# Kernel optimization log

Measured on AMD Instinct MI355X. Metric: run time of the kernel, lower is better.

## Reference

```python
import jax, jax.numpy as jnp
import numpy as np

N = 100000      # nodes
E = 1600000     # edges (avg degree 16)
D_IN, D_H, D_OUT = 128, 128, 64
NORM_SCALE = 1.0
EPS = 1e-6


def setup_inputs() -> dict:
    key = jax.random.key(0)
    ks = jax.random.split(key, 9)
    x = jax.random.normal(ks[0], (N, D_IN), dtype=jnp.float32)
    edge_index = jax.random.randint(ks[1], (2, E), 0, N, dtype=jnp.int32)
    edge_weight = jax.random.uniform(ks[2], (E,), dtype=jnp.float32)
    # GraphConv = Linear then spmm(adj, .); Glorot-ish init for weights
    W0 = jax.random.normal(ks[3], (D_IN, D_H), dtype=jnp.float32) / np.float32(np.sqrt(D_IN))
    b0 = jnp.zeros((D_H,), jnp.float32)
    W1 = jax.random.normal(ks[4], (D_H, D_H), dtype=jnp.float32) / np.float32(np.sqrt(D_H))
    b1 = jnp.zeros((D_H,), jnp.float32)
    Wout = jax.random.normal(ks[5], (D_H, D_OUT), dtype=jnp.float32) / np.float32(np.sqrt(D_H))
    bout = jnp.zeros((D_OUT,), jnp.float32)
    return {"x": x, "edge_index": edge_index, "edge_weight": edge_weight,
            "W0": W0, "b0": b0, "W1": W1, "b1": b1, "Wout": Wout, "bout": bout}


def _pair_norm(h):
    # PairNorm mode 'PN': center columns, divide by sqrt(mean squared row norm)
    h = h - jnp.mean(h, axis=0, keepdims=True)
    rownorm_mean = jnp.sqrt(EPS + jnp.mean(jnp.sum(h * h, axis=1)))
    return NORM_SCALE * h / rownorm_mean


def reference(x, edge_index, edge_weight, W0, b0, W1, b1, Wout, bout):
    src = edge_index[0]
    dst = edge_index[1]

    def graph_conv(h, W, b):
        h = h @ W + b                              # [N, d_out]
        msg = edge_weight[:, None] * h[src]        # [E, d_out] gather
        return jax.ops.segment_sum(msg, dst, num_segments=N)  # spmm(adj, h)

    x_old = jnp.zeros((), jnp.float32)
    for (W, b) in ((W0, b0), (W1, b1)):
        # dropout p=0 -> identity (omitted)
        h = graph_conv(x, W, b)
        h = jax.nn.relu(_pair_norm(h))
        x = h + x_old        # residual=1 -> skip every layer
        x_old = x
    return graph_conv(x, Wout, bout)
```

## Files before the change

### kernel.cpp

```cpp
#include <hip/hip_runtime.h>

#define N_NODES 100000
#define N_EDGES 1600000
#define DH 128
#define DOUT 64
#define EPS 1e-6f
#define NBINS 8
#define BINW 12500
#define NREP 64

typedef __attribute__((ext_vector_type(8))) short s8v;
typedef __attribute__((ext_vector_type(4))) float f32x4;

__device__ inline unsigned bfround(float f) {
    unsigned u = __float_as_uint(f);
    return (u + 0x7fffu + ((u >> 16) & 1u)) >> 16;
}
__device__ inline unsigned pack2(float a, float b) { return bfround(a) | (bfround(b) << 16); }
__device__ inline float blo(unsigned u) { return __uint_as_float(u << 16); }
__device__ inline float bhi(unsigned u) { return __uint_as_float(u & 0xffff0000u); }

template <int COLS, int PN>
__global__ __launch_bounds__(256) void gemm_mfma(const float* __restrict__ Xa,
                                                 const float* __restrict__ muA,
                                                 const float* __restrict__ invA,
                                                 const float* __restrict__ Xb,
                                                 const float* __restrict__ muB,
                                                 const float* __restrict__ invB,
                                                 const float* __restrict__ W,
                                                 const float* __restrict__ bias,
                                                 unsigned* __restrict__ Y, int nrows) {
    constexpr int CT = COLS / 16;
    __shared__ unsigned wtu[COLS][64];
    __shared__ unsigned xbu[64][64];

    const int tid = threadIdx.x;
    const int wv = tid >> 6;
    const int lane = tid & 63;
    const float sA = (PN >= 1) ? invA[0] : 0.f;
    const float sB = (PN == 2) ? invB[0] : 0.f;

    {
        ushort* wts = (ushort*)wtu;
        constexpr int NV4 = 128 * COLS / 4;
        for (int i = tid; i < NV4; i += 256) {
            int k = i / (COLS / 4);
            int c4 = i % (COLS / 4);
            float4 w4 = reinterpret_cast<const float4*>(W)[i];
            float vals[4] = {w4.x, w4.y, w4.z, w4.w};
            int u = k >> 1, kb = k & 1;
#pragma unroll
            for (int j = 0; j < 4; ++j) {
                int c = c4 * 4 + j;
                int us = u ^ ((c & 7) << 2);
                wts[c * 128 + us * 2 + kb] = (ushort)bfround(vals[j]);
            }
        }
    }

    float bv[CT];
#pragma unroll
    for (int f = 0; f < CT; ++f) bv[f] = bias[f * 16 + (lane & 15)];

    const int row0 = blockIdx.x * 128;
    const int myr = (wv << 4) + (lane & 15);

#pragma unroll
    for (int ms = 0; ms < 2; ++ms) {
        const int rb = row0 + ms * 64;
        __syncthreads();
        for (int i = tid; i < 2048; i += 256) {
            int r = i >> 5;
            int c4 = i & 31;
            float4 v = make_float4(0.f, 0.f, 0.f, 0.f);
            if (rb + r < nrows) {
                v = reinterpret_cast<const float4*>(Xa + (size_t)(rb + r) * 128)[c4];
                if constexpr (PN >= 1) {
                    float4 m = reinterpret_cast<const float4*>(muA)[c4];
                    v.x = fmaxf((v.x - m.x) * sA, 0.f);
                    v.y = fmaxf((v.y - m.y) * sA, 0.f);
                    v.z = fmaxf((v.z - m.z) * sA, 0.f);
                    v.w = fmaxf((v.w - m.w) * sA, 0.f);
                }
                if constexpr (PN == 2) {
                    float4 v2 = reinterpret_cast<const float4*>(Xb + (size_t)(rb + r) * 128)[c4];
                    float4 m2 = reinterpret_cast<const float4*>(muB)[c4];
                    v.x += fmaxf((v2.x - m2.x) * sB, 0.f);
                    v.y += fmaxf((v2.y - m2.y) * sB, 0.f);
                    v.z += fmaxf((v2.z - m2.z) * sB, 0.f);
                    v.w += fmaxf((v2.w - m2.w) * sB, 0.f);
                }
            }
            int sw = (r & 7) << 2;
            xbu[r][(c4 * 2) ^ sw] = pack2(v.x, v.y);
            xbu[r][(c4 * 2 + 1) ^ sw] = pack2(v.z, v.w);
        }
        __syncthreads();

        f32x4 acc[CT];
#pragma unroll
        for (int f = 0; f < CT; ++f) acc[f] = (f32x4){0.f, 0.f, 0.f, 0.f};
        const int xsw = (myr & 7) << 2;
#pragma unroll
        for (int kc = 0; kc < 4; ++kc) {
            const int u0 = kc * 16 + (lane >> 4) * 4;
            s8v a = *reinterpret_cast<const s8v*>(&xbu[myr][u0 ^ xsw]);
#pragma unroll
            for (int f = 0; f < CT; ++f) {
                const int c = f * 16 + (lane & 15);
                s8v b = *reinterpret_cast<const s8v*>(&wtu[c][u0 ^ ((c & 7) << 2)]);
                acc[f] = __builtin_amdgcn_mfma_f32_16x16x32_bf16(a, b, acc[f], 0, 0, 0);
            }
        }

#pragma unroll
        for (int f = 0; f < CT; ++f) {
#pragma unroll
            for (int r = 0; r < 4; ++r) {
                float v = acc[f][r] + bv[f];
                float p = __shfl_xor(v, 1, 64);
                unsigned pk = (lane & 1) ? pack2(p, v) : pack2(v, p);
                int grow = rb + (wv << 4) + ((lane >> 4) << 2) + r;
                if (grow < nrows && ((lane & 1) == (f & 1))) {
                    Y[(size_t)grow * (COLS / 2) + f * 8 + ((lane & 15) >> 1)] = pk;
                }
            }
        }
    }
}

__global__ __launch_bounds__(256) void hist_kernel(const int* __restrict__ dst,
                                                   int* __restrict__ counts) {
    int i = blockIdx.x * blockDim.x + threadIdx.x;
    const int stride = gridDim.x * blockDim.x;
    for (; i < N_EDGES / 4; i += stride) {
        int4 d = reinterpret_cast<const int4*>(dst)[i];
        atomicAdd(&counts[d.x], 1);
        atomicAdd(&counts[d.y], 1);
        atomicAdd(&counts[d.z], 1);
        atomicAdd(&counts[d.w], 1);
    }
}

__global__ __launch_bounds__(1024) void scan_kernel(const int* __restrict__ counts,
                                                    int* __restrict__ rowptr) {
    __shared__ int wsum[16];
    const int tid = threadIdx.x;
    const int lane = tid & 63;
    const int w = tid >> 6;
    int offset = 0;
    if (tid == 0) rowptr[0] = 0;
    for (int base = 0; base < N_NODES; base += 4096) {
        int i = base + tid * 4;
        int4 v = make_int4(0, 0, 0, 0);
        if (i < N_NODES) v = *reinterpret_cast<const int4*>(counts + i);
        int p0 = v.x, p1 = p0 + v.y, p2 = p1 + v.z, p3 = p2 + v.w;
        int incl = p3;
#pragma unroll
        for (int d = 1; d < 64; d <<= 1) {
            int t = __shfl_up(incl, d, 64);
            if (lane >= d) incl += t;
        }
        if (lane == 63) wsum[w] = incl;
        __syncthreads();
        if (w == 0 && lane < 16) {
            int t = wsum[lane];
#pragma unroll
            for (int d = 1; d < 16; d <<= 1) {
                int u = __shfl_up(t, d, 64);
                if (lane >= d) t += u;
            }
            wsum[lane] = t;
        }
        __syncthreads();
        int woff = (w == 0) ? 0 : wsum[w - 1];
        int chunk_total = wsum[15];
        int tbase = offset + woff + incl - p3;
        if (i < N_NODES) {
            rowptr[i + 1] = tbase + p0;
            rowptr[i + 2] = tbase + p1;
            rowptr[i + 3] = tbase + p2;
            rowptr[i + 4] = tbase + p3;
        }
        offset += chunk_total;
        __syncthreads();
    }
}

__global__ __launch_bounds__(256) void bucket_kernel(const int* __restrict__ src,
                                                     const int* __restrict__ dst,
                                                     const float* __restrict__ ew,
                                                     const int* __restrict__ rowptr,
                                                     int* __restrict__ fill,
                                                     int2* __restrict__ em) {
    const int myBin = blockIdx.x & (NBINS - 1);
    const int lo = myBin * BINW;
    const int hi = lo + BINW;
    int e = (blockIdx.x >> 3) * 256 + threadIdx.x;
    const int stride = (gridDim.x >> 3) * 256;
    for (; e < N_EDGES; e += stride) {
        int d = dst[e];
        if (d >= lo && d < hi) {
            int pos = atomicAdd(&fill[d], 1);
            em[rowptr[d] + pos] = make_int2(src[e], __float_as_int(ew[e]));
        }
    }
}

__global__ __launch_bounds__(256) void agg128b_kernel(const unsigned* __restrict__ Hb,
                                                      const int* __restrict__ rowptr,
                                                      const int2* __restrict__ em,
                                                      float* __restrict__ B,
                                                      float* __restrict__ cs_part,
                                                      float* __restrict__ ss_part) {
    __shared__ int2 smeta[4][64];
    __shared__ float cs[4][128];
    __shared__ float ssw[4];
    const int wv = threadIdx.x >> 6;
    const int lane = threadIdx.x & 63;
    const int node = blockIdx.x * 4 + wv;
    const int beg = rowptr[node];
    const int end = rowptr[node + 1];
    const int2* sm = smeta[wv];
    float ax0 = 0.f, ay0 = 0.f, ax1 = 0.f, ay1 = 0.f;

    for (int c = beg; c < end; c += 64) {
        smeta[wv][lane] = (c + lane < end) ? em[c + lane] : make_int2(0, 0);
        const int cnt = min(64, end - c);
        const int rounds = (cnt + 7) >> 3;
        for (int g = 0; g < rounds; ++g) {
            int2 m0 = sm[g * 8 + 0];
            int2 m1 = sm[g * 8 + 1];
            int2 m2 = sm[g * 8 + 2];
            int2 m3 = sm[g * 8 + 3];
            int2 m4 = sm[g * 8 + 4];
            int2 m5 = sm[g * 8 + 5];
            int2 m6 = sm[g * 8 + 6];
            int2 m7 = sm[g * 8 + 7];
            unsigned u0 = Hb[(size_t)m0.x * 64 + lane];
            unsigned u1 = Hb[(size_t)m1.x * 64 + lane];
            unsigned u2 = Hb[(size_t)m2.x * 64 + lane];
            unsigned u3 = Hb[(size_t)m3.x * 64 + lane];
            unsigned u4 = Hb[(size_t)m4.x * 64 + lane];
            unsigned u5 = Hb[(size_t)m5.x * 64 + lane];
            unsigned u6 = Hb[(size_t)m6.x * 64 + lane];
            unsigned u7 = Hb[(size_t)m7.x * 64 + lane];
            float w0 = __int_as_float(m0.y), w1 = __int_as_float(m1.y);
            float w2 = __int_as_float(m2.y), w3 = __int_as_float(m3.y);
            float w4 = __int_as_float(m4.y), w5 = __int_as_float(m5.y);
            float w6 = __int_as_float(m6.y), w7 = __int_as_float(m7.y);
            ax0 += w0 * blo(u0); ay0 += w0 * bhi(u0);
            ax1 += w1 * blo(u1); ay1 += w1 * bhi(u1);
            ax0 += w2 * blo(u2); ay0 += w2 * bhi(u2);
            ax1 += w3 * blo(u3); ay1 += w3 * bhi(u3);
            ax0 += w4 * blo(u4); ay0 += w4 * bhi(u4);
            ax1 += w5 * blo(u5); ay1 += w5 * bhi(u5);
            ax0 += w6 * blo(u6); ay0 += w6 * bhi(u6);
            ax1 += w7 * blo(u7); ay1 += w7 * bhi(u7);
        }
    }
    float2 acc = make_float2(ax0 + ax1, ay0 + ay1);
    reinterpret_cast<float2*>(B + (size_t)node * DH)[lane] = acc;

    cs[wv][lane * 2] = acc.x;
    cs[wv][lane * 2 + 1] = acc.y;
    float sq = acc.x * acc.x + acc.y * acc.y;
#pragma unroll
    for (int off = 32; off; off >>= 1) sq += __shfl_down(sq, off, 64);
    if (lane == 0) ssw[wv] = sq;
    __syncthreads();
    const int rep = blockIdx.x & (NREP - 1);
    if (threadIdx.x < 128) {
        float s = cs[0][threadIdx.x] + cs[1][threadIdx.x] + cs[2][threadIdx.x] + cs[3][threadIdx.x];
        atomicAdd(&cs_part[rep * 128 + threadIdx.x], s);
    }
    if (threadIdx.x == 0) atomicAdd(&ss_part[rep], ssw[0] + ssw[1] + ssw[2] + ssw[3]);
}

__global__ __launch_bounds__(256) void agg64b_kernel(const unsigned* __restrict__ Hb,
                                                     const int* __restrict__ rowptr,
                                                     const int2* __restrict__ em,
                                                     float* __restrict__ out) {
    __shared__ int2 smeta[4][64];
    const int wv = threadIdx.x >> 6;
    const int lane = threadIdx.x & 63;
    const int half = lane >> 5;
    const int col = lane & 31;
    const int node = blockIdx.x * 4 + wv;
    const int beg = rowptr[node];
    const int end = rowptr[node + 1];
    const int2* sm = smeta[wv];
    float ax0 = 0.f, ay0 = 0.f, ax1 = 0.f, ay1 = 0.f;

    for (int c = beg; c < end; c += 64) {
        smeta[wv][lane] = (c + lane < end) ? em[c + lane] : make_int2(0, 0);
        const int cnt = min(64, end - c);
        const int rounds = (cnt + 15) >> 4;
        for (int g = 0; g < rounds; ++g) {
            const int b = g * 16 + half;
            int2 m0 = sm[b + 0];
            int2 m1 = sm[b + 2];
            int2 m2 = sm[b + 4];
            int2 m3 = sm[b + 6];
            int2 m4 = sm[b + 8];
            int2 m5 = sm[b + 10];
            int2 m6 = sm[b + 12];
            int2 m7 = sm[b + 14];
            unsigned u0 = Hb[(size_t)m0.x * 32 + col];
            unsigned u1 = Hb[(size_t)m1.x * 32 + col];
            unsigned u2 = Hb[(size_t)m2.x * 32 + col];
            unsigned u3 = Hb[(size_t)m3.x * 32 + col];
            unsigned u4 = Hb[(size_t)m4.x * 32 + col];
            unsigned u5 = Hb[(size_t)m5.x * 32 + col];
            unsigned u6 = Hb[(size_t)m6.x * 32 + col];
            unsigned u7 = Hb[(size_t)m7.x * 32 + col];
            float w0 = __int_as_float(m0.y), w1 = __int_as_float(m1.y);
            float w2 = __int_as_float(m2.y), w3 = __int_as_float(m3.y);
            float w4 = __int_as_float(m4.y), w5 = __int_as_float(m5.y);
            float w6 = __int_as_float(m6.y), w7 = __int_as_float(m7.y);
            ax0 += w0 * blo(u0); ay0 += w0 * bhi(u0);
            ax1 += w1 * blo(u1); ay1 += w1 * bhi(u1);
            ax0 += w2 * blo(u2); ay0 += w2 * bhi(u2);
            ax1 += w3 * blo(u3); ay1 += w3 * bhi(u3);
            ax0 += w4 * blo(u4); ay0 += w4 * bhi(u4);
            ax1 += w5 * blo(u5); ay1 += w5 * bhi(u5);
            ax0 += w6 * blo(u6); ay0 += w6 * bhi(u6);
            ax1 += w7 * blo(u7); ay1 += w7 * bhi(u7);
        }
    }
    float ax = ax0 + ax1, ay = ay0 + ay1;
    ax += __shfl_xor(ax, 32, 64);
    ay += __shfl_xor(ay, 32, 64);
    if (lane < 32) {
        reinterpret_cast<float2*>(out + (size_t)node * DOUT)[col] = make_float2(ax, ay);
    }
}

__global__ void finalize_stats(const float* __restrict__ cs_part,
                               const float* __restrict__ ss_part, float* __restrict__ mu,
                               float* __restrict__ inv) {
    const int t = threadIdx.x;
    float m = 0.f;
    for (int r = 0; r < NREP; ++r) m += cs_part[r * 128 + t];
    float mean = m / (float)N_NODES;
    mu[t] = mean;
    float v = mean * mean;
    __shared__ float partl[2];
    __shared__ float sstot;
#pragma unroll
    for (int off = 32; off; off >>= 1) v += __shfl_down(v, off, 64);
    if ((t & 63) == 0) partl[t >> 6] = v;
    float ss = (t < NREP) ? ss_part[t] : 0.f;
#pragma unroll
    for (int off = 32; off; off >>= 1) ss += __shfl_down(ss, off, 64);
    if (t == 0) sstot = ss;
    __syncthreads();
    if (t == 0) {
        float musq = partl[0] + partl[1];
        float s = (sstot - (float)N_NODES * musq) / (float)N_NODES;
        inv[0] = rsqrtf(EPS + s);
    }
}

extern "C" void kernel_launch(void* const* d_in, const int* in_sizes, int n_in,
                              void* d_out, int out_size, void* d_ws, size_t ws_size,
                              hipStream_t stream) {
    const float* x = (const float*)d_in[0];
    const int* edge_index = (const int*)d_in[1];
    const float* ew = (const float*)d_in[2];
    const float* W0 = (const float*)d_in[3];
    const float* b0 = (const float*)d_in[4];
    const float* W1 = (const float*)d_in[5];
    const float* b1 = (const float*)d_in[6];
    const float* Wout = (const float*)d_in[7];
    const float* bout = (const float*)d_in[8];

    const int* src = edge_index;
    const int* dst = edge_index + N_EDGES;
    float* out = (float*)d_out;

    float* base = (float*)d_ws;
    unsigned* Hb = (unsigned*)base;
    float* B1 = base + (size_t)N_NODES * 64;
    float* B2 = B1 + (size_t)N_NODES * DH;
    int2* em = (int2*)(B2 + (size_t)N_NODES * DH);
    int* counts = (int*)(em + N_EDGES);
    int* fill = counts + N_NODES;
    int* rowptr = fill + N_NODES;
    size_t soff = (size_t)(rowptr + N_NODES + 1 - (int*)base);
    soff = (soff + 3) & ~(size_t)3;
    float* stats = base + soff;
    float* cs_part1 = stats;
    float* ss_part1 = cs_part1 + NREP * 128;
    float* cs_part2 = ss_part1 + NREP;
    float* ss_part2 = cs_part2 + NREP * 128;
    float* mu1 = ss_part2 + NREP;
    float* inv1 = mu1 + 128;
    float* mu2 = inv1 + 4;
    float* inv2 = mu2 + 128;

    const int gemm_grid = (N_NODES + 127) / 128;
    const int agg_grid = N_NODES / 4;

    hipMemsetAsync(counts, 0, (size_t)2 * N_NODES * sizeof(int), stream);
    hipMemsetAsync(stats, 0, (size_t)2 * (NREP * 128 + NREP) * sizeof(float), stream);

    hist_kernel<<<1024, 256, 0, stream>>>(dst, counts);
    scan_kernel<<<1, 1024, 0, stream>>>(counts, rowptr);
    bucket_kernel<<<2048, 256, 0, stream>>>(src, dst, ew, rowptr, fill, em);

    gemm_mfma<128, 0><<<gemm_grid, 256, 0, stream>>>(
        x, nullptr, nullptr, nullptr, nullptr, nullptr, W0, b0, Hb, N_NODES);
    agg128b_kernel<<<agg_grid, 256, 0, stream>>>(Hb, rowptr, em, B1, cs_part1, ss_part1);
    finalize_stats<<<1, 128, 0, stream>>>(cs_part1, ss_part1, mu1, inv1);

    gemm_mfma<128, 1><<<gemm_grid, 256, 0, stream>>>(
        B1, mu1, inv1, nullptr, nullptr, nullptr, W1, b1, Hb, N_NODES);
    agg128b_kernel<<<agg_grid, 256, 0, stream>>>(Hb, rowptr, em, B2, cs_part2, ss_part2);
    finalize_stats<<<1, 128, 0, stream>>>(cs_part2, ss_part2, mu2, inv2);

    gemm_mfma<64, 2><<<gemm_grid, 256, 0, stream>>>(
        B2, mu2, inv2, B1, mu1, inv1, Wout, bout, Hb, N_NODES);
    agg64b_kernel<<<agg_grid, 256, 0, stream>>>(Hb, rowptr, em, out);
}
```

Baseline: 556.7 us.

## Store aggregated hidden features as bf16 and widen gather loads in aggregation kernels

The intermediate aggregation outputs B1/B2 are now written as packed bf16 instead of fp32, and the following GEMMs read bf16 and unpack them while applying PairNorm. This halves the bytes written by the 128-wide aggregation and read back by the next GEMMs. The aggregation kernels also switch to 8-byte uint2 gathers, so each lane handles four columns and the edge list is split across wave halves or quarters, followed by a shuffle reduction. The cost is extra rounding of intermediates to bf16, with slightly lower accuracy, and per-node stats are still computed from the fp32 accumulators.

After: 539.4 us. 1.03x faster.

```diff
diff --git a/kernel.cpp b/kernel.cpp
--- a/kernel.cpp
+++ b/kernel.cpp
@@ -21,10 +21,10 @@
 __device__ inline float bhi(unsigned u) { return __uint_as_float(u & 0xffff0000u); }
 
 template <int COLS, int PN>
-__global__ __launch_bounds__(256) void gemm_mfma(const float* __restrict__ Xa,
+__global__ __launch_bounds__(256) void gemm_mfma(const void* __restrict__ Xav,
                                                  const float* __restrict__ muA,
                                                  const float* __restrict__ invA,
-                                                 const float* __restrict__ Xb,
+                                                 const unsigned* __restrict__ Xbu2,
                                                  const float* __restrict__ muB,
                                                  const float* __restrict__ invB,
                                                  const float* __restrict__ W,
@@ -69,31 +69,56 @@
     for (int ms = 0; ms < 2; ++ms) {
         const int rb = row0 + ms * 64;
         __syncthreads();
-        for (int i = tid; i < 2048; i += 256) {
-            int r = i >> 5;
-            int c4 = i & 31;
-            float4 v = make_float4(0.f, 0.f, 0.f, 0.f);
-            if (rb + r < nrows) {
-                v = reinterpret_cast<const float4*>(Xa + (size_t)(rb + r) * 128)[c4];
-                if constexpr (PN >= 1) {
-                    float4 m = reinterpret_cast<const float4*>(muA)[c4];
-                    v.x = fmaxf((v.x - m.x) * sA, 0.f);
-                    v.y = fmaxf((v.y - m.y) * sA, 0.f);
-                    v.z = fmaxf((v.z - m.z) * sA, 0.f);
-                    v.w = fmaxf((v.w - m.w) * sA, 0.f);
+        if constexpr (PN == 0) {
+            const float* Xa = (const float*)Xav;
+            for (int i = tid; i < 2048; i += 256) {
+                int r = i >> 5;
+                int c4 = i & 31;
+                float4 v = make_float4(0.f, 0.f, 0.f, 0.f);
+                if (rb + r < nrows) v = reinterpret_cast<const float4*>(Xa + (size_t)(rb + r) * 128)[c4];
+                int sw = (r & 7) << 2;
+                xbu[r][(c4 * 2) ^ sw] = pack2(v.x, v.y);
+                xbu[r][(c4 * 2 + 1) ^ sw] = pack2(v.z, v.w);
+            }
+        } else {
+            const unsigned* Xa = (const unsigned*)Xav;
+            for (int i = tid; i < 1024; i += 256) {
+                int r = i >> 4;
+                int c4 = i & 15;
+                float v0 = 0.f, v1 = 0.f, v2 = 0.f, v3 = 0.f, v4 = 0.f, v5 = 0.f, v6 = 0.f,
+                      v7 = 0.f;
+                if (rb + r < nrows) {
+                    uint4 uv = reinterpret_cast<const uint4*>(Xa + (size_t)(rb + r) * 64)[c4];
+                    float4 ma = reinterpret_cast<const float4*>(muA)[c4 * 2];
+                    float4 mb = reinterpret_cast<const float4*>(muA)[c4 * 2 + 1];
+                    v0 = fmaxf((blo(uv.x) - ma.x) * sA, 0.f);
+                    v1 = fmaxf((bhi(uv.x) - ma.y) * sA, 0.f);
+                    v2 = fmaxf((blo(uv.y) - ma.z) * sA, 0.f);
+                    v3 = fmaxf((bhi(uv.y) - ma.w) * sA, 0.f);
+                    v4 = fmaxf((blo(uv.z) - mb.x) * sA, 0.f);
+                    v5 = fmaxf((bhi(uv.z) - mb.y) * sA, 0.f);
+                    v6 = fmaxf((blo(uv.w) - mb.z) * sA, 0.f);
+                    v7 = fmaxf((bhi(uv.w) - mb.w) * sA, 0.f);
+                    if constexpr (PN == 2) {
+                        uint4 u2 = reinterpret_cast<const uint4*>(Xbu2 + (size_t)(rb + r) * 64)[c4];
+                        float4 na = reinterpret_cast<const float4*>(muB)[c4 * 2];
+                        float4 nb = reinterpret_cast<const float4*>(muB)[c4 * 2 + 1];
+                        v0 += fmaxf((blo(u2.x) - na.x) * sB, 0.f);
+                        v1 += fmaxf((bhi(u2.x) - na.y) * sB, 0.f);
+                        v2 += fmaxf((blo(u2.y) - na.z) * sB, 0.f);
+                        v3 += fmaxf((bhi(u2.y) - na.w) * sB, 0.f);
+                        v4 += fmaxf((blo(u2.z) - nb.x) * sB, 0.f);
+                        v5 += fmaxf((bhi(u2.z) - nb.y) * sB, 0.f);
+                        v6 += fmaxf((blo(u2.w) - nb.z) * sB, 0.f);
+                        v7 += fmaxf((bhi(u2.w) - nb.w) * sB, 0.f);
+                    }
                 }
-                if constexpr (PN == 2) {
-                    float4 v2 = reinterpret_cast<const float4*>(Xb + (size_t)(rb + r) * 128)[c4];
-                    float4 m2 = reinterpret_cast<const float4*>(muB)[c4];
-                    v.x += fmaxf((v2.x - m2.x) * sB, 0.f);
-                    v.y += fmaxf((v2.y - m2.y) * sB, 0.f);
-                    v.z += fmaxf((v2.z - m2.z) * sB, 0.f);
-                    v.w += fmaxf((v2.w - m2.w) * sB, 0.f);
-                }
-            }
-            int sw = (r & 7) << 2;
-            xbu[r][(c4 * 2) ^ sw] = pack2(v.x, v.y);
-            xbu[r][(c4 * 2 + 1) ^ sw] = pack2(v.z, v.w);
+                int sw = (r & 7) << 2;
+                xbu[r][(c4 * 4 + 0) ^ sw] = pack2(v0, v1);
+                xbu[r][(c4 * 4 + 1) ^ sw] = pack2(v2, v3);
+                xbu[r][(c4 * 4 + 2) ^ sw] = pack2(v4, v5);
+                xbu[r][(c4 * 4 + 3) ^ sw] = pack2(v6, v7);
+            }
         }
         __syncthreads();
 
@@ -210,7 +235,7 @@
 __global__ __launch_bounds__(256) void agg128b_kernel(const unsigned* __restrict__ Hb,
                                                       const int* __restrict__ rowptr,
                                                       const int2* __restrict__ em,
-                                                      float* __restrict__ B,
+                                                      unsigned* __restrict__ Bb,
                                                       float* __restrict__ cs_part,
                                                       float* __restrict__ ss_part) {
     __shared__ int2 smeta[4][64];
@@ -218,79 +243,13 @@
     __shared__ float ssw[4];
     const int wv = threadIdx.x >> 6;
     const int lane = threadIdx.x & 63;
+    const int half = lane >> 5;
+    const int col2 = lane & 31;
     const int node = blockIdx.x * 4 + wv;
     const int beg = rowptr[node];
     const int end = rowptr[node + 1];
     const int2* sm = smeta[wv];
-    float ax0 = 0.f, ay0 = 0.f, ax1 = 0.f, ay1 = 0.f;
-
-    for (int c = beg; c < end; c += 64) {
-        smeta[wv][lane] = (c + lane < end) ? em[c + lane] : make_int2(0, 0);
-        const int cnt = min(64, end - c);
-        const int rounds = (cnt + 7) >> 3;
-        for (int g = 0; g < rounds; ++g) {
-            int2 m0 = sm[g * 8 + 0];
-            int2 m1 = sm[g * 8 + 1];
-            int2 m2 = sm[g * 8 + 2];
-            int2 m3 = sm[g * 8 + 3];
-            int2 m4 = sm[g * 8 + 4];
-            int2 m5 = sm[g * 8 + 5];
-            int2 m6 = sm[g * 8 + 6];
-            int2 m7 = sm[g * 8 + 7];
-            unsigned u0 = Hb[(size_t)m0.x * 64 + lane];
-            unsigned u1 = Hb[(size_t)m1.x * 64 + lane];
-            unsigned u2 = Hb[(size_t)m2.x * 64 + lane];
-            unsigned u3 = Hb[(size_t)m3.x * 64 + lane];
-            unsigned u4 = Hb[(size_t)m4.x * 64 + lane];
-            unsigned u5 = Hb[(size_t)m5.x * 64 + lane];
-            unsigned u6 = Hb[(size_t)m6.x * 64 + lane];
-            unsigned u7 = Hb[(size_t)m7.x * 64 + lane];
-            float w0 = __int_as_float(m0.y), w1 = __int_as_float(m1.y);
-            float w2 = __int_as_float(m2.y), w3 = __int_as_float(m3.y);
-            float w4 = __int_as_float(m4.y), w5 = __int_as_float(m5.y);
-            float w6 = __int_as_float(m6.y), w7 = __int_as_float(m7.y);
-            ax0 += w0 * blo(u0); ay0 += w0 * bhi(u0);
-            ax1 += w1 * blo(u1); ay1 += w1 * bhi(u1);
-            ax0 += w2 * blo(u2); ay0 += w2 * bhi(u2);
-            ax1 += w3 * blo(u3); ay1 += w3 * bhi(u3);
-            ax0 += w4 * blo(u4); ay0 += w4 * bhi(u4);
-            ax1 += w5 * blo(u5); ay1 += w5 * bhi(u5);
-            ax0 += w6 * blo(u6); ay0 += w6 * bhi(u6);
-            ax1 += w7 * blo(u7); ay1 += w7 * bhi(u7);
-        }
-    }
-    float2 acc = make_float2(ax0 + ax1, ay0 + ay1);
-    reinterpret_cast<float2*>(B + (size_t)node * DH)[lane] = acc;
-
-    cs[wv][lane * 2] = acc.x;
-    cs[wv][lane * 2 + 1] = acc.y;
-    float sq = acc.x * acc.x + acc.y * acc.y;
-#pragma unroll
-    for (int off = 32; off; off >>= 1) sq += __shfl_down(sq, off, 64);
-    if (lane == 0) ssw[wv] = sq;
-    __syncthreads();
-    const int rep = blockIdx.x & (NREP - 1);
-    if (threadIdx.x < 128) {
-        float s = cs[0][threadIdx.x] + cs[1][threadIdx.x] + cs[2][threadIdx.x] + cs[3][threadIdx.x];
-        atomicAdd(&cs_part[rep * 128 + threadIdx.x], s);
-    }
-    if (threadIdx.x == 0) atomicAdd(&ss_part[rep], ssw[0] + ssw[1] + ssw[2] + ssw[3]);
-}
-
-__global__ __launch_bounds__(256) void agg64b_kernel(const unsigned* __restrict__ Hb,
-                                                     const int* __restrict__ rowptr,
-                                                     const int2* __restrict__ em,
-                                                     float* __restrict__ out) {
-    __shared__ int2 smeta[4][64];
-    const int wv = threadIdx.x >> 6;
-    const int lane = threadIdx.x & 63;
-    const int half = lane >> 5;
-    const int col = lane & 31;
-    const int node = blockIdx.x * 4 + wv;
-    const int beg = rowptr[node];
-    const int end = rowptr[node + 1];
-    const int2* sm = smeta[wv];
-    float ax0 = 0.f, ay0 = 0.f, ax1 = 0.f, ay1 = 0.f;
+    float a0 = 0.f, a1 = 0.f, a2 = 0.f, a3 = 0.f;
 
     for (int c = beg; c < end; c += 64) {
         smeta[wv][lane] = (c + lane < end) ? em[c + lane] : make_int2(0, 0);
@@ -306,33 +265,115 @@
             int2 m5 = sm[b + 10];
             int2 m6 = sm[b + 12];
             int2 m7 = sm[b + 14];
-            unsigned u0 = Hb[(size_t)m0.x * 32 + col];
-            unsigned u1 = Hb[(size_t)m1.x * 32 + col];
-            unsigned u2 = Hb[(size_t)m2.x * 32 + col];
-            unsigned u3 = Hb[(size_t)m3.x * 32 + col];
-            unsigned u4 = Hb[(size_t)m4.x * 32 + col];
-            unsigned u5 = Hb[(size_t)m5.x * 32 + col];
-            unsigned u6 = Hb[(size_t)m6.x * 32 + col];
-            unsigned u7 = Hb[(size_t)m7.x * 32 + col];
+            uint2 u0 = *reinterpret_cast<const uint2*>(Hb + (size_t)m0.x * 64 + col2 * 2);
+            uint2 u1 = *reinterpret_cast<const uint2*>(Hb + (size_t)m1.x * 64 + col2 * 2);
+            uint2 u2 = *reinterpret_cast<const uint2*>(Hb + (size_t)m2.x * 64 + col2 * 2);
+            uint2 u3 = *reinterpret_cast<const uint2*>(Hb + (size_t)m3.x * 64 + col2 * 2);
+            uint2 u4 = *reinterpret_cast<const uint2*>(Hb + (size_t)m4.x * 64 + col2 * 2);
+            uint2 u5 = *reinterpret_cast<const uint2*>(Hb + (size_t)m5.x * 64 + col2 * 2);
+            uint2 u6 = *reinterpret_cast<const uint2*>(Hb + (size_t)m6.x * 64 + col2 * 2);
+            uint2 u7 = *reinterpret_cast<const uint2*>(Hb + (size_t)m7.x * 64 + col2 * 2);
             float w0 = __int_as_float(m0.y), w1 = __int_as_float(m1.y);
             float w2 = __int_as_float(m2.y), w3 = __int_as_float(m3.y);
             float w4 = __int_as_float(m4.y), w5 = __int_as_float(m5.y);
             float w6 = __int_as_float(m6.y), w7 = __int_as_float(m7.y);
-            ax0 += w0 * blo(u0); ay0 += w0 * bhi(u0);
-            ax1 += w1 * blo(u1); ay1 += w1 * bhi(u1);
-            ax0 += w2 * blo(u2); ay0 += w2 * bhi(u2);
-            ax1 += w3 * blo(u3); ay1 += w3 * bhi(u3);
-            ax0 += w4 * blo(u4); ay0 += w4 * bhi(u4);
-            ax1 += w5 * blo(u5); ay1 += w5 * bhi(u5);
-            ax0 += w6 * blo(u6); ay0 += w6 * bhi(u6);
-            ax1 += w7 * blo(u7); ay1 += w7 * bhi(u7);
-        }
-    }
-    float ax = ax0 + ax1, ay = ay0 + ay1;
-    ax += __shfl_xor(ax, 32, 64);
-    ay += __shfl_xor(ay, 32, 64);
+            a0 += w0 * blo(u0.x); a1 += w0 * bhi(u0.x); a2 += w0 * blo(u0.y); a3 += w0 * bhi(u0.y);
+            a0 += w1 * blo(u1.x); a1 += w1 * bhi(u1.x); a2 += w1 * blo(u1.y); a3 += w1 * bhi(u1.y);
+            a0 += w2 * blo(u2.x); a1 += w2 * bhi(u2.x); a2 += w2 * blo(u2.y); a3 += w2 * bhi(u2.y);
+            a0 += w3 * blo(u3.x); a1 += w3 * bhi(u3.x); a2 += w3 * blo(u3.y); a3 += w3 * bhi(u3.y);
+            a0 += w4 * blo(u4.x); a1 += w4 * bhi(u4.x); a2 += w4 * blo(u4.y); a3 += w4 * bhi(u4.y);
+            a0 += w5 * blo(u5.x); a1 += w5 * bhi(u5.x); a2 += w5 * blo(u5.y); a3 += w5 * bhi(u5.y);
+            a0 += w6 * blo(u6.x); a1 += w6 * bhi(u6.x); a2 += w6 * blo(u6.y); a3 += w6 * bhi(u6.y);
+            a0 += w7 * blo(u7.x); a1 += w7 * bhi(u7.x); a2 += w7 * blo(u7.y); a3 += w7 * bhi(u7.y);
+        }
+    }
+    a0 += __shfl_xor(a0, 32, 64);
+    a1 += __shfl_xor(a1, 32, 64);
+    a2 += __shfl_xor(a2, 32, 64);
+    a3 += __shfl_xor(a3, 32, 64);
+
+    float sq = 0.f;
     if (lane < 32) {
-        reinterpret_cast<float2*>(out + (size_t)node * DOUT)[col] = make_float2(ax, ay);
+        uint2 op;
+        op.x = pack2(a0, a1);
+        op.y = pack2(a2, a3);
+        *reinterpret_cast<uint2*>(Bb + (size_t)node * 64 + col2 * 2) = op;
+        cs[wv][col2 * 4 + 0] = a0;
+        cs[wv][col2 * 4 + 1] = a1;
+        cs[wv][col2 * 4 + 2] = a2;
+        cs[wv][col2 * 4 + 3] = a3;
+        sq = a0 * a0 + a1 * a1 + a2 * a2 + a3 * a3;
+    }
+#pragma unroll
+    for (int off = 32; off; off >>= 1) sq += __shfl_down(sq, off, 64);
+    if (lane == 0) ssw[wv] = sq;
+    __syncthreads();
+    const int rep = blockIdx.x & (NREP - 1);
+    if (threadIdx.x < 128) {
+        float s = cs[0][threadIdx.x] + cs[1][threadIdx.x] + cs[2][threadIdx.x] + cs[3][threadIdx.x];
+        atomicAdd(&cs_part[rep * 128 + threadIdx.x], s);
+    }
+    if (threadIdx.x == 0) atomicAdd(&ss_part[rep], ssw[0] + ssw[1] + ssw[2] + ssw[3]);
+}
+
+__global__ __launch_bounds__(256) void agg64b_kernel(const unsigned* __restrict__ Hb,
+                                                     const int* __restrict__ rowptr,
+                                                     const int2* __restrict__ em,
+                                                     float* __restrict__ out) {
+    __shared__ int2 smeta[4][64];
+    const int wv = threadIdx.x >> 6;
+    const int lane = threadIdx.x & 63;
+    const int q = lane >> 4;
+    const int col2 = lane & 15;
+    const int node = blockIdx.x * 4 + wv;
+    const int beg = rowptr[node];
+    const int end = rowptr[node + 1];
+    const int2* sm = smeta[wv];
+    float a0 = 0.f, a1 = 0.f, a2 = 0.f, a3 = 0.f;
+
+    for (int c = beg; c < end; c += 64) {
+        smeta[wv][lane] = (c + lane < end) ? em[c + lane] : make_int2(0, 0);
+        const int cnt = min(64, end - c);
+        const int rounds = (cnt + 31) >> 5;
+        for (int g = 0; g < rounds; ++g) {
+            const int b = g * 32 + q;
+            int2 m0 = sm[b + 0];
+            int2 m1 = sm[b + 4];
+            int2 m2 = sm[b + 8];
+            int2 m3 = sm[b + 12];
+            int2 m4 = sm[b + 16];
+            int2 m5 = sm[b + 20];
+            int2 m6 = sm[b + 24];
+            int2 m7 = sm[b + 28];
+            uint2 u0 = *reinterpret_cast<const uint2*>(Hb + (size_t)m0.x * 32 + col2 * 2);
+            uint2 u1 = *reinterpret_cast<const uint2*>(Hb + (size_t)m1.x * 32 + col2 * 2);
+            uint2 u2 = *reinterpret_cast<const uint2*>(Hb + (size_t)m2.x * 32 + col2 * 2);
+            uint2 u3 = *reinterpret_cast<const uint2*>(Hb + (size_t)m3.x * 32 + col2 * 2);
+            uint2 u4 = *reinterpret_cast<const uint2*>(Hb + (size_t)m4.x * 32 + col2 * 2);
+            uint2 u5 = *reinterpret_cast<const uint2*>(Hb + (size_t)m5.x * 32 + col2 * 2);
+            uint2 u6 = *reinterpret_cast<const uint2*>(Hb + (size_t)m6.x * 32 + col2 * 2);
+            uint2 u7 = *reinterpret_cast<const uint2*>(Hb + (size_t)m7.x * 32 + col2 * 2);
+            float w0 = __int_as_float(m0.y), w1 = __int_as_float(m1.y);
+            float w2 = __int_as_float(m2.y), w3 = __int_as_float(m3.y);
+            float w4 = __int_as_float(m4.y), w5 = __int_as_float(m5.y);
+            float w6 = __int_as_float(m6.y), w7 = __int_as_float(m7.y);
+            a0 += w0 * blo(u0.x); a1 += w0 * bhi(u0.x); a2 += w0 * blo(u0.y); a3 += w0 * bhi(u0.y);
+            a0 += w1 * blo(u1.x); a1 += w1 * bhi(u1.x); a2 += w1 * blo(u1.y); a3 += w1 * bhi(u1.y);
+            a0 += w2 * blo(u2.x); a1 += w2 * bhi(u2.x); a2 += w2 * blo(u2.y); a3 += w2 * bhi(u2.y);
+            a0 += w3 * blo(u3.x); a1 += w3 * bhi(u3.x); a2 += w3 * blo(u3.y); a3 += w3 * bhi(u3.y);
+            a0 += w4 * blo(u4.x); a1 += w4 * bhi(u4.x); a2 += w4 * blo(u4.y); a3 += w4 * bhi(u4.y);
+            a0 += w5 * blo(u5.x); a1 += w5 * bhi(u5.x); a2 += w5 * blo(u5.y); a3 += w5 * bhi(u5.y);
+            a0 += w6 * blo(u6.x); a1 += w6 * bhi(u6.x); a2 += w6 * blo(u6.y); a3 += w6 * bhi(u6.y);
+            a0 += w7 * blo(u7.x); a1 += w7 * bhi(u7.x); a2 += w7 * blo(u7.y); a3 += w7 * bhi(u7.y);
+        }
+    }
+    a0 += __shfl_xor(a0, 16, 64); a0 += __shfl_xor(a0, 32, 64);
+    a1 += __shfl_xor(a1, 16, 64); a1 += __shfl_xor(a1, 32, 64);
+    a2 += __shfl_xor(a2, 16, 64); a2 += __shfl_xor(a2, 32, 64);
+    a3 += __shfl_xor(a3, 16, 64); a3 += __shfl_xor(a3, 32, 64);
+    if (lane < 16) {
+        *reinterpret_cast<float4*>(out + (size_t)node * DOUT + col2 * 4) =
+            make_float4(a0, a1, a2, a3);
     }
 }
 
@@ -379,17 +420,17 @@
     const int* dst = edge_index + N_EDGES;
     float* out = (float*)d_out;
 
-    float* base = (float*)d_ws;
-    unsigned* Hb = (unsigned*)base;
-    float* B1 = base + (size_t)N_NODES * 64;
-    float* B2 = B1 + (size_t)N_NODES * DH;
-    int2* em = (int2*)(B2 + (size_t)N_NODES * DH);
+    unsigned* base = (unsigned*)d_ws;
+    unsigned* Hb = base;
+    unsigned* B1b = base + (size_t)N_NODES * 64;
+    unsigned* B2b = B1b + (size_t)N_NODES * 64;
+    int2* em = (int2*)(B2b + (size_t)N_NODES * 64);
     int* counts = (int*)(em + N_EDGES);
     int* fill = counts + N_NODES;
     int* rowptr = fill + N_NODES;
     size_t soff = (size_t)(rowptr + N_NODES + 1 - (int*)base);
     soff = (soff + 3) & ~(size_t)3;
-    float* stats = base + soff;
+    float* stats = (float*)base + soff;
     float* cs_part1 = stats;
     float* ss_part1 = cs_part1 + NREP * 128;
     float* cs_part2 = ss_part1 + NREP;
@@ -411,15 +452,15 @@
 
     gemm_mfma<128, 0><<<gemm_grid, 256, 0, stream>>>(
         x, nullptr, nullptr, nullptr, nullptr, nullptr, W0, b0, Hb, N_NODES);
-    agg128b_kernel<<<agg_grid, 256, 0, stream>>>(Hb, rowptr, em, B1, cs_part1, ss_part1);
+    agg128b_kernel<<<agg_grid, 256, 0, stream>>>(Hb, rowptr, em, B1b, cs_part1, ss_part1);
     finalize_stats<<<1, 128, 0, stream>>>(cs_part1, ss_part1, mu1, inv1);
 
     gemm_mfma<128, 1><<<gemm_grid, 256, 0, stream>>>(
-        B1, mu1, inv1, nullptr, nullptr, nullptr, W1, b1, Hb, N_NODES);
-    agg128b_kernel<<<agg_grid, 256, 0, stream>>>(Hb, rowptr, em, B2, cs_part2, ss_part2);
+        B1b, mu1, inv1, nullptr, nullptr, nullptr, W1, b1, Hb, N_NODES);
+    agg128b_kernel<<<agg_grid, 256, 0, stream>>>(Hb, rowptr, em, B2b, cs_part2, ss_part2);
     finalize_stats<<<1, 128, 0, stream>>>(cs_part2, ss_part2, mu2, inv2);
 
     gemm_mfma<64, 2><<<gemm_grid, 256, 0, stream>>>(
-        B2, mu2, inv2, B1, mu1, inv1, Wout, bout, Hb, N_NODES);
+        B2b, mu2, inv2, B1b, mu1, inv1, Wout, bout, Hb, N_NODES);
     agg64b_kernel<<<agg_grid, 256, 0, stream>>>(Hb, rowptr, em, out);
 }
```
